# Kernel tuning notes

Hardware: AMD Instinct MI355X
Metric: run time of the kernel (lower is better)

Reference implementation:

```python
import jax, jax.numpy as jnp
import numpy as np

B, S, D, H = 2, 2048, 1024, 16
HD = D // H  # 64
MASK_VAL = -10000.0


def setup_inputs() -> dict:
    key = jax.random.key(0)
    ks = jax.random.split(key, 8)
    sc = 0.02
    q_features = jax.random.normal(ks[0], (B, S, D), jnp.float32)
    kv_features = jax.random.normal(ks[1], (B, S, D), jnp.float32)
    # causal mask, broadcastable (1,1,S,S)
    mask = jnp.tril(jnp.ones((S, S), jnp.bool_))[None, None]
    Wq = jax.random.normal(ks[2], (D, D), jnp.float32) * sc
    bq = jnp.zeros((D,), jnp.float32)
    Wkv = jax.random.normal(ks[3], (D, 2 * D), jnp.float32) * sc
    bkv = jnp.zeros((2 * D,), jnp.float32)
    Wp = jax.random.normal(ks[4], (D, D), jnp.float32) * sc
    bp = jnp.zeros((D,), jnp.float32)
    return {"q_features": q_features, "kv_features": kv_features, "mask": mask,
            "Wq": Wq, "bq": bq, "Wkv": Wkv, "bkv": bkv, "Wp": Wp, "bp": bp}


def _split_heads(t):
    # (B,S,D) -> (B,H,S,HD)
    return t.reshape(B, S, H, HD).transpose(0, 2, 1, 3)


def reference(q_features, kv_features, mask, Wq, bq, Wkv, bkv, Wp, bp):
    query = q_features @ Wq + bq            # (B,S,D)
    kv = kv_features @ Wkv + bkv            # (B,S,2D)
    key, value = jnp.split(kv, 2, axis=-1)
    q = _split_heads(query)                 # (B,H,S,HD)
    k = _split_heads(key)
    v = _split_heads(value)
    scores = jnp.einsum('bhqd,bhkd->bhqk', q, k) / jnp.sqrt(jnp.float32(HD))
    scores = jnp.where(mask, scores, jnp.asarray(MASK_VAL, scores.dtype))
    attn = jax.nn.softmax(scores, axis=-1)  # (B,H,S,S)
    out = jnp.einsum('bhqk,bhkd->bhqd', attn, v)
    out = out.transpose(0, 2, 1, 3).reshape(B, S, D)  # merge heads
    return out @ Wp + bp
```

## Files before the change

kernel.cpp:

```cpp
#include <hip/hip_runtime.h>

typedef unsigned short u16;
typedef unsigned int u32;
typedef __attribute__((ext_vector_type(4))) unsigned short us4;
typedef __attribute__((ext_vector_type(8))) unsigned short us8;
typedef __attribute__((ext_vector_type(4))) short s16x4;
typedef __attribute__((ext_vector_type(8))) __bf16 bf16x8;
typedef __attribute__((ext_vector_type(4))) float floatx4;

#define S_ 2048
#define D_ 1024
#define QSC 0.18033688f

__device__ __forceinline__ float b2f(u16 u) {
  unsigned v = ((unsigned)u) << 16;
  return __builtin_bit_cast(float, v);
}
__device__ __forceinline__ u16 f2bf(float f) {
  unsigned u = __builtin_bit_cast(unsigned, f);
  unsigned r = (u + 0x7fffu + ((u >> 16) & 1u)) >> 16;
  return (u16)r;
}
__device__ __forceinline__ u16 f2bf_rhu(float f) {
  return (u16)((__builtin_bit_cast(unsigned, f) + 0x8000u) >> 16);
}

typedef const __attribute__((address_space(1))) u32* gas_t;
typedef __attribute__((address_space(3))) u32* las_t;
__device__ __forceinline__ void gload16(const u16* g, u16* l) {
  __builtin_amdgcn_global_load_lds((gas_t)g, (las_t)l, 16, 0, 0);
}

#define PBAR()                                   \
  {                                              \
    __builtin_amdgcn_sched_barrier(0);           \
    asm volatile("" ::: "memory");               \
    __builtin_amdgcn_s_barrier();                \
    asm volatile("" ::: "memory");               \
    __builtin_amdgcn_sched_barrier(0);           \
  }
#define WAITVM(N) asm volatile("s_waitcnt vmcnt(" #N ")" ::: "memory")

__global__ __launch_bounds__(256) void prep(
    const float* __restrict__ qf, const float* __restrict__ kvf,
    const float* __restrict__ Wq, const float* __restrict__ Wkv,
    const float* __restrict__ Wp, u16* __restrict__ qa, u16* __restrict__ kva,
    u16* __restrict__ Wqt, u16* __restrict__ Wkvt, u16* __restrict__ Wpt) {
  int bid = blockIdx.x, tid = threadIdx.x;
  if (bid < 4096) {
    const float* src = (bid < 2048) ? qf : kvf;
    u16* dst = (bid < 2048) ? qa : kva;
    size_t i = ((size_t)(bid & 2047) * 256 + tid) * 8;
    floatx4 a = *(const floatx4*)(src + i);
    floatx4 b = *(const floatx4*)(src + i + 4);
    us8 r;
#pragma unroll
    for (int j = 0; j < 4; j++) { r[j] = f2bf(a[j]); r[4 + j] = f2bf(b[j]); }
    *(us8*)(dst + i) = r;
  } else {
    int t = bid - 4096;
    const float* src; u16* dst; int R, C;
    if (t < 1024)      { src = Wq;  dst = Wqt;  R = 1024; C = 1024; }
    else if (t < 3072) { t -= 1024; src = Wkv; dst = Wkvt; R = 1024; C = 2048; }
    else               { t -= 3072; src = Wp;  dst = Wpt;  R = 1024; C = 1024; }
    int bx = t % (C >> 5), by = t / (C >> 5);
    __shared__ u16 tile[32][33];
    int tx = tid & 31, ty = tid >> 5;
    int x = bx * 32 + tx;
    for (int i = ty; i < 32; i += 8)
      tile[i][tx] = f2bf(src[(size_t)(by * 32 + i) * C + x]);
    __syncthreads();
    int ox = by * 32 + tx;
    for (int i = ty; i < 32; i += 8)
      dst[(size_t)(bx * 32 + i) * R + ox] = tile[tx][i];
  }
}

template <int MODE>
__device__ __forceinline__ void gemm256(
    const u16* __restrict__ A, const u16* __restrict__ Bt,
    const float* __restrict__ bias, void* __restrict__ C0,
    u16* __restrict__ C1, int N, int m0, int n0, u16* smem, float cscale) {
  int tid = threadIdx.x;
  int w = tid >> 6, lane = tid & 63;
  int quad = lane >> 4, l16 = lane & 15;
  int wr = w >> 2, wc = w & 3;

  int gch = ((lane & 7) ^ ((lane >> 3) & 7)) << 3;
  const u16* Ag = A + (size_t)(m0 + w * 32 + (lane >> 3)) * 1024 + gch;
  const u16* Bg = Bt + (size_t)(n0 + w * 32 + (lane >> 3)) * 1024 + gch;
  u16* Adst = smem + w * 32 * 64;
  u16* Bdst = smem + 32768 + w * 32 * 64;

  int ab = (wr * 128 + l16) * 64;
  int bb = 32768 + (wc * 64 + l16) * 64;
  int xk0 = (quad ^ (l16 & 7)) << 3;
  int xk1 = ((4 + quad) ^ (l16 & 7)) << 3;

  floatx4 acc[8][4] = {};

#define STAGE3(tn, SD)                                                  \
  {                                                                     \
    _Pragma("unroll") for (int i = 0; i < 4; i++) {                     \
      gload16(Ag + (size_t)(tn) * 64 + (size_t)i * 8192,                \
              Adst + (SD) + i * 512);                                   \
      gload16(Bg + (size_t)(tn) * 64 + (size_t)i * 8192,                \
              Bdst + (SD) + i * 512);                                   \
    }                                                                   \
  }

#define COMPUTE3(SOFF)                                                  \
  {                                                                     \
    _Pragma("unroll") for (int kk = 0; kk < 2; kk++) {                  \
      int xk = kk ? xk1 : xk0;                                          \
      bf16x8 bfr[4];                                                    \
      _Pragma("unroll") for (int nf = 0; nf < 4; nf++)                  \
        bfr[nf] = __builtin_bit_cast(bf16x8,                            \
            *(const us8*)&smem[(SOFF) + bb + nf * 1024 + xk]);          \
      _Pragma("unroll") for (int mf = 0; mf < 8; mf++) {                \
        bf16x8 afr = __builtin_bit_cast(bf16x8,                         \
            *(const us8*)&smem[(SOFF) + ab + mf * 1024 + xk]);          \
        _Pragma("unroll") for (int nf = 0; nf < 4; nf++)                \
          acc[mf][nf] = __builtin_amdgcn_mfma_f32_16x16x32_bf16(        \
              afr, bfr[nf], acc[mf][nf], 0, 0, 0);                      \
      }                                                                 \
    }                                                                   \
  }

  STAGE3(0, 0);
  WAITVM(0);
  PBAR();
#pragma unroll 1
  for (int t = 0; t < 16; t += 2) {
    STAGE3(t + 1, 16384);
    COMPUTE3(0);
    WAITVM(0);
    PBAR();
    if (t + 2 < 16) STAGE3(t + 2, 0);
    COMPUTE3(16384);
    WAITVM(0);
    PBAR();
  }

#undef STAGE3
#undef COMPUTE3

#pragma unroll
  for (int mf = 0; mf < 8; mf++) {
#pragma unroll
    for (int nf = 0; nf < 4; nf++) {
      int col = n0 + wc * 64 + nf * 16 + l16;
      int rowq = m0 + wr * 128 + mf * 16 + quad * 4;
      float bv = bias[col];
      if (MODE == 0) {
        u16* o = (u16*)C0;
#pragma unroll
        for (int r = 0; r < 4; r++)
          o[(size_t)(rowq + r) * N + col] = f2bf((acc[mf][nf][r] + bv) * cscale);
      } else {
        if (col < 1024) {
          u16* o = (u16*)C0;
#pragma unroll
          for (int r = 0; r < 4; r++)
            o[(size_t)(rowq + r) * 1024 + col] = f2bf(acc[mf][nf][r] + bv);
        } else {
          int vcol = col - 1024;
          int b = rowq >> 11, s0 = rowq & 2047;
          us4 pv;
#pragma unroll
          for (int r = 0; r < 4; r++) pv[r] = f2bf(acc[mf][nf][r] + bv);
          *(us4*)&C1[((size_t)(b * 1024 + vcol)) * (size_t)S_ + s0] = pv;
        }
      }
    }
  }
}

__global__ __launch_bounds__(512, 2) void gemm_qkv(
    const u16* __restrict__ qa, const u16* __restrict__ kva,
    const u16* __restrict__ Wqt, const u16* __restrict__ Wkvt,
    const float* __restrict__ bq, const float* __restrict__ bkv,
    u16* __restrict__ Qb, u16* __restrict__ Kb, u16* __restrict__ Vt) {
  __shared__ __align__(16) u16 smem[65536];
  int bid = blockIdx.x;
  int work = (bid & 7) * 24 + (bid >> 3);
  if (work < 64) {
    gemm256<0>(qa, Wqt, bq, Qb, nullptr, 1024,
               (work >> 2) * 256, (work & 3) * 256, smem, QSC);
  } else {
    int lb = work - 64;
    gemm256<2>(kva, Wkvt, bkv, Kb, Vt, 2048,
               (lb >> 3) * 256, (lb & 7) * 256, smem, 1.0f);
  }
}

template <int TM, int TN, int MODE>
__device__ __forceinline__ void gemm_core(
    const u16* __restrict__ A, const u16* __restrict__ Bt,
    const float* __restrict__ bias, void* __restrict__ C0,
    u16* __restrict__ C1, int N, int n0, int m0,
    u16* As, u16* Bs, float cscale) {
  constexpr int MT = TM / 32, NT = TN / 32;
  int tid  = threadIdx.x;
  int wave = tid >> 6, lane = tid & 63;
  int quad = lane >> 4, l16 = lane & 15;
  int wr = wave >> 1, wc = wave & 1;
  const u16* Ag = A  + (size_t)(m0 + wave * 8 + (lane >> 3)) * 1024 + (lane & 7) * 8;
  const u16* Bg = Bt + (size_t)(n0 + wave * 8 + (lane >> 3)) * 1024 + (lane & 7) * 8;
  u16* Aw = As + wave * 8 * 64;
  u16* Bw = Bs + wave * 8 * 64;
  floatx4 acc[MT][NT] = {};
  for (int k0 = 0; k0 < 1024; k0 += 64) {
    if (k0) __syncthreads();
#pragma unroll
    for (int p = 0; p < TM / 32; p++)
      gload16(Ag + (size_t)p * 32 * 1024 + k0, Aw + p * 32 * 64);
#pragma unroll
    for (int p = 0; p < TN / 32; p++)
      gload16(Bg + (size_t)p * 32 * 1024 + k0, Bw + p * 32 * 64);
    __syncthreads();
#pragma unroll
    for (int kk = 0; kk < 2; kk++) {
      bf16x8 af[MT], bf[NT];
#pragma unroll
      for (int mt = 0; mt < MT; mt++)
        af[mt] = __builtin_bit_cast(bf16x8,
            *(const us8*)&As[(wr * (TM / 2) + mt * 16 + l16) * 64 + (kk * 4 + quad) * 8]);
#pragma unroll
      for (int nt = 0; nt < NT; nt++)
        bf[nt] = __builtin_bit_cast(bf16x8,
            *(const us8*)&Bs[(wc * (TN / 2) + nt * 16 + l16) * 64 + (kk * 4 + quad) * 8]);
#pragma unroll
      for (int mt = 0; mt < MT; mt++)
#pragma unroll
        for (int nt = 0; nt < NT; nt++)
          acc[mt][nt] = __builtin_amdgcn_mfma_f32_16x16x32_bf16(
              af[mt], bf[nt], acc[mt][nt], 0, 0, 0);
    }
  }
#pragma unroll
  for (int mt = 0; mt < MT; mt++) {
#pragma unroll
    for (int nt = 0; nt < NT; nt++) {
      int col  = n0 + wc * (TN / 2) + nt * 16 + l16;
      int rowq = m0 + wr * (TM / 2) + mt * 16 + quad * 4;
      float bv = bias[col];
      if (MODE == 0) {
        u16* o = (u16*)C0;
#pragma unroll
        for (int r = 0; r < 4; r++)
          o[(size_t)(rowq + r) * N + col] = f2bf((acc[mt][nt][r] + bv) * cscale);
      } else if (MODE == 1) {
        float* o = (float*)C0;
#pragma unroll
        for (int r = 0; r < 4; r++)
          o[(size_t)(rowq + r) * N + col] = acc[mt][nt][r] + bv;
      } else {
        if (col < 1024) {
          u16* o = (u16*)C0;
#pragma unroll
          for (int r = 0; r < 4; r++)
            o[(size_t)(rowq + r) * 1024 + col] = f2bf(acc[mt][nt][r] + bv);
        } else {
          int vcol = col - 1024;
          int b = rowq >> 11, s0 = rowq & 2047;
          us4 pv;
#pragma unroll
          for (int r = 0; r < 4; r++) pv[r] = f2bf(acc[mt][nt][r] + bv);
          *(us4*)&C1[((size_t)(b * 1024 + vcol)) * (size_t)S_ + s0] = pv;
        }
      }
    }
  }
}

__global__ __launch_bounds__(256) void gemm_out(
    const u16* __restrict__ AO, const u16* __restrict__ Wpt,
    const float* __restrict__ bp, float* __restrict__ out) {
  __shared__ __align__(16) u16 As[64 * 64];
  __shared__ __align__(16) u16 Bs[128 * 64];
  int work = (blockIdx.x & 7) * 64 + (blockIdx.x >> 3);
  gemm_core<64, 128, 1>(AO, Wpt, bp, out, nullptr, 1024,
                        (work & 7) * 128, (work >> 3) * 64, As, Bs, 1.0f);
}

__global__ __launch_bounds__(512) void attn_fwd(
    const u16* __restrict__ Q, const u16* __restrict__ Kb,
    const u16* __restrict__ Vt, u16* __restrict__ O,
    u16* __restrict__ Opart, float* __restrict__ ml) {
  __shared__ __align__(16) u16 sm[16384];
  int tid  = threadIdx.x;
  int w    = tid >> 6, lane = tid & 63;
  int quad = lane >> 4, l16 = lane & 15;
  int bh = blockIdx.x, b = bh >> 4, h = bh & 15;
  int y = blockIdx.y;

  static const signed char yt_[24] = {15,15,7,14,14,13,13,6,12,12,11,11,5,
                                      10,10,9,9,4,8,8,3,2,1,0};
  static const signed char yh_[24] = {0,1,-1,0,1,0,1,-1,0,1,0,1,-1,
                                      0,1,0,1,-1,0,1,-1,-1,-1,-1};
  int t = yt_[y], hh = yh_[y];
  bool split = hh >= 0;
  int kb0, kb1;
  if (split) { kb0 = hh ? (t + 1) : 0; kb1 = hh ? (2 * t + 2) : (t + 1); }
  else       { kb0 = 0; kb1 = 2 * t + 2; }
  int n = kb1 - kb0;

  const size_t row0 = (size_t)b * S_;
  const u16* Kg = Kb + row0 * D_ + h * 64;
  const u16* Vg = Vt + ((size_t)b * 1024 + h * 64) * S_;

  int qlo = t * 128 + w * 16;
  int dkb = qlo >> 6;
  int qg  = (qlo & 63) + l16;

  const u16* qp = Q + (row0 + qlo + l16) * D_ + h * 64 + quad * 8;
  bf16x8 aqv[2];
  aqv[0] = __builtin_bit_cast(bf16x8, *(const us8*)(qp));
  aqv[1] = __builtin_bit_cast(bf16x8, *(const us8*)(qp + 32));

  floatx4 o_[4] = {};
  floatx4 l_acc = {};
  const s16x4 ones4 = {0x3F80, 0x3F80, 0x3F80, 0x3F80};

  int srow = tid >> 3, c8 = tid & 7;
  int woff = srow * 64 + ((c8 ^ (srow & 7)) << 3);
  u16* smK = sm;
  u16* smV = sm + 8192;

  const u16* Kp = Kg + (size_t)(kb0 * 64 + srow) * D_ + c8 * 8;
  const u16* Vp = Vg + (size_t)srow * S_ + kb0 * 64 + c8 * 8;
  us8 pk = *(const us8*)Kp, pv = *(const us8*)Vp;
  *(us8*)&smK[woff] = pk;
  *(us8*)&smV[woff] = pv;
  if (n > 1) {
    Kp += (size_t)64 * D_; Vp += 64;
    pk = *(const us8*)Kp; pv = *(const us8*)Vp;
  }
  __syncthreads();

  for (int i = 0; i < n; i++) {
    int cur = i & 1;
    int kb = kb0 + i;
    if (i + 1 < n) {
      int nxt = (cur ^ 1) * 4096;
      *(us8*)&smK[nxt + woff] = pk;
      *(us8*)&smV[nxt + woff] = pv;
      if (i + 2 < n) {
        Kp += (size_t)64 * D_; Vp += 64;
        pk = *(const us8*)Kp; pv = *(const us8*)Vp;
      }
    }
    if (kb <= dkb) {
      const u16* Ksb = smK + cur * 4096;
      const u16* Vsb = smV + cur * 4096;

      floatx4 s[4] = {};
      __builtin_amdgcn_s_setprio(1);
#pragma unroll
      for (int kk = 0; kk < 2; kk++)
#pragma unroll
        for (int nt = 0; nt < 4; nt++) {
          us8 kf = *(const us8*)&Ksb[(nt * 16 + l16) * 64 +
                                     (((kk * 4 + quad) ^ (l16 & 7)) << 3)];
          s[nt] = __builtin_amdgcn_mfma_f32_16x16x32_bf16(
              __builtin_bit_cast(bf16x8, kf), aqv[kk], s[nt], 0, 0, 0);
        }
      __builtin_amdgcn_s_setprio(0);

      if (kb == dkb) {
#pragma unroll
        for (int nt = 0; nt < 4; nt++)
#pragma unroll
          for (int r = 0; r < 4; r++)
            if (nt * 16 + quad * 4 + r > qg) s[nt][r] = -1e5f;
      }

      s16x4 pb[4];
#pragma unroll
      for (int nt = 0; nt < 4; nt++)
#pragma unroll
        for (int r = 0; r < 4; r++)
          pb[nt][r] = (short)f2bf_rhu(__builtin_amdgcn_exp2f(s[nt][r]));

      __builtin_amdgcn_s_setprio(1);
#pragma unroll
      for (int nt = 0; nt < 4; nt++) {
        l_acc = __builtin_amdgcn_mfma_f32_16x16x16bf16_1k(ones4, pb[nt], l_acc, 0, 0, 0);
#pragma unroll
        for (int mt = 0; mt < 4; mt++) {
          int hd = mt * 16 + l16;
          int chunk = nt * 2 + (quad >> 1);
          us4 vf = *(const us4*)&Vsb[hd * 64 + ((chunk ^ (l16 & 7)) << 3) + (quad & 1) * 4];
          o_[mt] = __builtin_amdgcn_mfma_f32_16x16x16bf16_1k(
              __builtin_bit_cast(s16x4, vf), pb[nt], o_[mt], 0, 0, 0);
        }
      }
      __builtin_amdgcn_s_setprio(0);
    }
    __syncthreads();
  }

  if (!split) {
    float rl = __builtin_amdgcn_rcpf(l_acc[0]);
    size_t orow = (row0 + qlo + l16) * D_ + h * 64;
#pragma unroll
    for (int mt = 0; mt < 4; mt++) {
      us4 ov;
#pragma unroll
      for (int r = 0; r < 4; r++) ov[r] = f2bf(o_[mt][r] * rl);
      *(us4*)&O[orow + mt * 16 + quad * 4] = ov;
    }
  } else {
    int part = (t - 8) * 2 + hh;
    u16* op = Opart + ((size_t)(bh * 16 + part)) * 8192;
    int rloc = w * 16 + l16;
#pragma unroll
    for (int mt = 0; mt < 4; mt++) {
      us4 ov;
#pragma unroll
      for (int r = 0; r < 4; r++) ov[r] = f2bf(o_[mt][r]);
      *(us4*)&op[rloc * 64 + mt * 16 + quad * 4] = ov;
    }
    if (quad == 0)
      ml[(size_t)(bh * 16 + part) * 128 + rloc] = l_acc[0];
  }
}

__global__ __launch_bounds__(256) void combine(
    const u16* __restrict__ Opart, const float* __restrict__ ml,
    u16* __restrict__ O) {
  int bh = blockIdx.x, b = bh >> 4, h = bh & 15;
  int t = 8 + blockIdx.y;
  int p0 = bh * 16 + (t - 8) * 2;
  const u16* o1 = Opart + (size_t)p0 * 8192;
  const u16* o2 = o1 + 8192;
  int row = threadIdx.x >> 1, ch = (threadIdx.x & 1) * 32;
  float l1 = ml[(size_t)p0 * 128 + row];
  float l2 = ml[(size_t)(p0 + 1) * 128 + row];
  float inv = __builtin_amdgcn_rcpf(l1 + l2);
  size_t orow = ((size_t)b * S_ + t * 128 + row) * D_ + h * 64 + ch;
#pragma unroll
  for (int v = 0; v < 4; v++) {
    us8 x1 = *(const us8*)&o1[row * 64 + ch + v * 8];
    us8 x2 = *(const us8*)&o2[row * 64 + ch + v * 8];
    us8 out;
#pragma unroll
    for (int j = 0; j < 8; j++)
      out[j] = f2bf((b2f(x1[j]) + b2f(x2[j])) * inv);
    *(us8*)&O[orow + v * 8] = out;
  }
}

extern "C" void kernel_launch(void* const* d_in, const int* in_sizes, int n_in,
                              void* d_out, int out_size, void* d_ws, size_t ws_size,
                              hipStream_t stream) {
  const float* qf  = (const float*)d_in[0];
  const float* kvf = (const float*)d_in[1];
  const float* Wq  = (const float*)d_in[3];
  const float* bq  = (const float*)d_in[4];
  const float* Wkv = (const float*)d_in[5];
  const float* bkv = (const float*)d_in[6];
  const float* Wp  = (const float*)d_in[7];
  const float* bp  = (const float*)d_in[8];

  char* ws = (char*)d_ws;
  const size_t MB = 1048576;
  u16*   kva  = (u16*)(ws);
  u16*   AO   = (u16*)(ws);
  u16*   Kbp  = (u16*)(ws + 8 * MB);
  u16*   Vtp  = (u16*)(ws + 16 * MB);
  u16*   Wqt  = (u16*)(ws + 24 * MB);
  float* mlp  = (float*)(ws + 24 * MB);
  u16*   Wkvt = (u16*)(ws + 26 * MB);
  u16*   Wpt  = (u16*)(ws + 30 * MB);
  u16*   qa    = (u16*)d_out;
  u16*   Opart = (u16*)d_out;
  u16*   Qb    = (u16*)d_out + (size_t)4 * 1048576;

  prep<<<8192, 256, 0, stream>>>(qf, kvf, Wq, Wkv, Wp, qa, kva, Wqt, Wkvt, Wpt);
  gemm_qkv<<<192, 512, 0, stream>>>(qa, kva, Wqt, Wkvt, bq, bkv, Qb, Kbp, Vtp);
  attn_fwd<<<dim3(32, 24), 512, 0, stream>>>(Qb, Kbp, Vtp, AO, Opart, mlp);
  combine<<<dim3(32, 8), 256, 0, stream>>>(Opart, mlp, AO);
  gemm_out<<<512, 256, 0, stream>>>(AO, Wpt, bp, (float*)d_out);
}
```

Measured before the change: 211.0 us.

## Use 4-wave double-buffered swizzled GEMM with smaller tiles for QKV and output

Replaces the 256x256 8-wave QKV GEMM with a templated 4-wave 128x128 double-buffered swizzled kernel, which gives 768 blocks instead of 192 so more CUs are busy. The output projection moves from the simple single-buffered gemm_core to the same pipelined kernel with 128x64 tiles. The weight transpose in prep now writes 4-element vector stores. Smaller tiles reduce data reuse per block and raise global traffic, in exchange for better occupancy and load balance.

```diff
diff --git a/kernel.cpp b/kernel.cpp
--- a/kernel.cpp
+++ b/kernel.cpp
@@ -70,93 +70,103 @@
     for (int i = ty; i < 32; i += 8)
       tile[i][tx] = f2bf(src[(size_t)(by * 32 + i) * C + x]);
     __syncthreads();
-    int ox = by * 32 + tx;
-    for (int i = ty; i < 32; i += 8)
-      dst[(size_t)(bx * 32 + i) * R + ox] = tile[tx][i];
-  }
-}
-
-template <int MODE>
-__device__ __forceinline__ void gemm256(
+    int r = tid >> 3, c4 = tid & 7;
+    us4 v;
+#pragma unroll
+    for (int j = 0; j < 4; j++) v[j] = tile[c4 * 4 + j][r];
+    *(us4*)&dst[(size_t)(bx * 32 + r) * R + by * 32 + c4 * 4] = v;
+  }
+}
+
+template <int TM, int TN, int MODE>
+__device__ __forceinline__ void gemm4w(
     const u16* __restrict__ A, const u16* __restrict__ Bt,
     const float* __restrict__ bias, void* __restrict__ C0,
     u16* __restrict__ C1, int N, int m0, int n0, u16* smem, float cscale) {
+  constexpr int MF = TM / 32, NF = TN / 32;
+  constexpr int ASZ = TM * 64;
+  constexpr int SLOT = (TM + TN) * 64;
   int tid = threadIdx.x;
   int w = tid >> 6, lane = tid & 63;
   int quad = lane >> 4, l16 = lane & 15;
-  int wr = w >> 2, wc = w & 3;
+  int wr = w >> 1, wc = w & 1;
 
   int gch = ((lane & 7) ^ ((lane >> 3) & 7)) << 3;
-  const u16* Ag = A + (size_t)(m0 + w * 32 + (lane >> 3)) * 1024 + gch;
-  const u16* Bg = Bt + (size_t)(n0 + w * 32 + (lane >> 3)) * 1024 + gch;
-  u16* Adst = smem + w * 32 * 64;
-  u16* Bdst = smem + 32768 + w * 32 * 64;
-
-  int ab = (wr * 128 + l16) * 64;
-  int bb = 32768 + (wc * 64 + l16) * 64;
+  const u16* Ag = A + (size_t)(m0 + w * (TM / 4) + (lane >> 3)) * 1024 + gch;
+  const u16* Bg = Bt + (size_t)(n0 + w * (TN / 4) + (lane >> 3)) * 1024 + gch;
+  u16* Adst = smem + w * (TM / 4) * 64;
+  u16* Bdst = smem + ASZ + w * (TN / 4) * 64;
+
+  int ab = (wr * (TM / 2) + l16) * 64;
+  int bb = ASZ + (wc * (TN / 2) + l16) * 64;
   int xk0 = (quad ^ (l16 & 7)) << 3;
   int xk1 = ((4 + quad) ^ (l16 & 7)) << 3;
 
-  floatx4 acc[8][4] = {};
-
-#define STAGE3(tn, SD)                                                  \
+  floatx4 acc[MF][NF] = {};
+
+#define STAGE4(tn, s_)                                                  \
   {                                                                     \
-    _Pragma("unroll") for (int i = 0; i < 4; i++) {                     \
+    _Pragma("unroll") for (int i = 0; i < MF; i++)                      \
       gload16(Ag + (size_t)(tn) * 64 + (size_t)i * 8192,                \
-              Adst + (SD) + i * 512);                                   \
+              Adst + (s_) * SLOT + i * 512);                            \
+    _Pragma("unroll") for (int i = 0; i < NF; i++)                      \
       gload16(Bg + (size_t)(tn) * 64 + (size_t)i * 8192,                \
-              Bdst + (SD) + i * 512);                                   \
-    }                                                                   \
-  }
-
-#define COMPUTE3(SOFF)                                                  \
+              Bdst + (s_) * SLOT + i * 512);                            \
+  }
+
+#define COMPUTE4(SOFF)                                                  \
   {                                                                     \
     _Pragma("unroll") for (int kk = 0; kk < 2; kk++) {                  \
       int xk = kk ? xk1 : xk0;                                          \
-      bf16x8 bfr[4];                                                    \
-      _Pragma("unroll") for (int nf = 0; nf < 4; nf++)                  \
+      bf16x8 bfr[NF];                                                   \
+      _Pragma("unroll") for (int nf = 0; nf < NF; nf++)                 \
         bfr[nf] = __builtin_bit_cast(bf16x8,                            \
             *(const us8*)&smem[(SOFF) + bb + nf * 1024 + xk]);          \
-      _Pragma("unroll") for (int mf = 0; mf < 8; mf++) {                \
+      _Pragma("unroll") for (int mf = 0; mf < MF; mf++) {               \
         bf16x8 afr = __builtin_bit_cast(bf16x8,                         \
             *(const us8*)&smem[(SOFF) + ab + mf * 1024 + xk]);          \
-        _Pragma("unroll") for (int nf = 0; nf < 4; nf++)                \
+        _Pragma("unroll") for (int nf = 0; nf < NF; nf++)               \
           acc[mf][nf] = __builtin_amdgcn_mfma_f32_16x16x32_bf16(        \
               afr, bfr[nf], acc[mf][nf], 0, 0, 0);                      \
       }                                                                 \
     }                                                                   \
   }
 
-  STAGE3(0, 0);
+  STAGE4(0, 0);
   WAITVM(0);
   PBAR();
 #pragma unroll 1
   for (int t = 0; t < 16; t += 2) {
-    STAGE3(t + 1, 16384);
-    COMPUTE3(0);
+    STAGE4(t + 1, 1);
+    COMPUTE4(0);
     WAITVM(0);
     PBAR();
-    if (t + 2 < 16) STAGE3(t + 2, 0);
-    COMPUTE3(16384);
+    if (t + 2 < 16) STAGE4(t + 2, 0);
+    COMPUTE4(SLOT);
     WAITVM(0);
     PBAR();
   }
 
-#undef STAGE3
-#undef COMPUTE3
-
-#pragma unroll
-  for (int mf = 0; mf < 8; mf++) {
-#pragma unroll
-    for (int nf = 0; nf < 4; nf++) {
-      int col = n0 + wc * 64 + nf * 16 + l16;
-      int rowq = m0 + wr * 128 + mf * 16 + quad * 4;
+#undef STAGE4
+#undef COMPUTE4
+
+#pragma unroll
+  for (int mf = 0; mf < MF; mf++) {
+#pragma unroll
+    for (int nf = 0; nf < NF; nf++) {
+      int col = n0 + wc * (TN / 2) + nf * 16 + l16;
+      int rowq = m0 + wr * (TM / 2) + mf * 16 + quad * 4;
       float bv = bias[col];
       if (MODE == 0) {
         u16* o = (u16*)C0;
 #pragma unroll
         for (int r = 0; r < 4; r++)
           o[(size_t)(rowq + r) * N + col] = f2bf((acc[mf][nf][r] + bv) * cscale);
+      } else if (MODE == 1) {
+        float* o = (float*)C0;
+#pragma unroll
+        for (int r = 0; r < 4; r++)
+          o[(size_t)(rowq + r) * N + col] = acc[mf][nf][r] + bv;
       } else {
         if (col < 1024) {
           u16* o = (u16*)C0;
@@ -176,112 +186,31 @@
   }
 }
 
-__global__ __launch_bounds__(512, 2) void gemm_qkv(
+__global__ __launch_bounds__(256, 2) void gemm_qkv(
     const u16* __restrict__ qa, const u16* __restrict__ kva,
     const u16* __restrict__ Wqt, const u16* __restrict__ Wkvt,
     const float* __restrict__ bq, const float* __restrict__ bkv,
     u16* __restrict__ Qb, u16* __restrict__ Kb, u16* __restrict__ Vt) {
-  __shared__ __align__(16) u16 smem[65536];
+  __shared__ __align__(16) u16 smem[32768];
   int bid = blockIdx.x;
-  int work = (bid & 7) * 24 + (bid >> 3);
-  if (work < 64) {
-    gemm256<0>(qa, Wqt, bq, Qb, nullptr, 1024,
-               (work >> 2) * 256, (work & 3) * 256, smem, QSC);
+  int work = (bid & 7) * 96 + (bid >> 3);
+  if (work < 256) {
+    gemm4w<128, 128, 0>(qa, Wqt, bq, Qb, nullptr, 1024,
+                        (work >> 3) * 128, (work & 7) * 128, smem, QSC);
   } else {
-    int lb = work - 64;
-    gemm256<2>(kva, Wkvt, bkv, Kb, Vt, 2048,
-               (lb >> 3) * 256, (lb & 7) * 256, smem, 1.0f);
-  }
-}
-
-template <int TM, int TN, int MODE>
-__device__ __forceinline__ void gemm_core(
-    const u16* __restrict__ A, const u16* __restrict__ Bt,
-    const float* __restrict__ bias, void* __restrict__ C0,
-    u16* __restrict__ C1, int N, int n0, int m0,
-    u16* As, u16* Bs, float cscale) {
-  constexpr int MT = TM / 32, NT = TN / 32;
-  int tid  = threadIdx.x;
-  int wave = tid >> 6, lane = tid & 63;
-  int quad = lane >> 4, l16 = lane & 15;
-  int wr = wave >> 1, wc = wave & 1;
-  const u16* Ag = A  + (size_t)(m0 + wave * 8 + (lane >> 3)) * 1024 + (lane & 7) * 8;
-  const u16* Bg = Bt + (size_t)(n0 + wave * 8 + (lane >> 3)) * 1024 + (lane & 7) * 8;
-  u16* Aw = As + wave * 8 * 64;
-  u16* Bw = Bs + wave * 8 * 64;
-  floatx4 acc[MT][NT] = {};
-  for (int k0 = 0; k0 < 1024; k0 += 64) {
-    if (k0) __syncthreads();
-#pragma unroll
-    for (int p = 0; p < TM / 32; p++)
-      gload16(Ag + (size_t)p * 32 * 1024 + k0, Aw + p * 32 * 64);
-#pragma unroll
-    for (int p = 0; p < TN / 32; p++)
-      gload16(Bg + (size_t)p * 32 * 1024 + k0, Bw + p * 32 * 64);
-    __syncthreads();
-#pragma unroll
-    for (int kk = 0; kk < 2; kk++) {
-      bf16x8 af[MT], bf[NT];
-#pragma unroll
-      for (int mt = 0; mt < MT; mt++)
-        af[mt] = __builtin_bit_cast(bf16x8,
-            *(const us8*)&As[(wr * (TM / 2) + mt * 16 + l16) * 64 + (kk * 4 + quad) * 8]);
-#pragma unroll
-      for (int nt = 0; nt < NT; nt++)
-        bf[nt] = __builtin_bit_cast(bf16x8,
-            *(const us8*)&Bs[(wc * (TN / 2) + nt * 16 + l16) * 64 + (kk * 4 + quad) * 8]);
-#pragma unroll
-      for (int mt = 0; mt < MT; mt++)
-#pragma unroll
-        for (int nt = 0; nt < NT; nt++)
-          acc[mt][nt] = __builtin_amdgcn_mfma_f32_16x16x32_bf16(
-              af[mt], bf[nt], acc[mt][nt], 0, 0, 0);
-    }
-  }
-#pragma unroll
-  for (int mt = 0; mt < MT; mt++) {
-#pragma unroll
-    for (int nt = 0; nt < NT; nt++) {
-      int col  = n0 + wc * (TN / 2) + nt * 16 + l16;
-      int rowq = m0 + wr * (TM / 2) + mt * 16 + quad * 4;
-      float bv = bias[col];
-      if (MODE == 0) {
-        u16* o = (u16*)C0;
-#pragma unroll
-        for (int r = 0; r < 4; r++)
-          o[(size_t)(rowq + r) * N + col] = f2bf((acc[mt][nt][r] + bv) * cscale);
-      } else if (MODE == 1) {
-        float* o = (float*)C0;
-#pragma unroll
-        for (int r = 0; r < 4; r++)
-          o[(size_t)(rowq + r) * N + col] = acc[mt][nt][r] + bv;
-      } else {
-        if (col < 1024) {
-          u16* o = (u16*)C0;
-#pragma unroll
-          for (int r = 0; r < 4; r++)
-            o[(size_t)(rowq + r) * 1024 + col] = f2bf(acc[mt][nt][r] + bv);
-        } else {
-          int vcol = col - 1024;
-          int b = rowq >> 11, s0 = rowq & 2047;
-          us4 pv;
-#pragma unroll
-          for (int r = 0; r < 4; r++) pv[r] = f2bf(acc[mt][nt][r] + bv);
-          *(us4*)&C1[((size_t)(b * 1024 + vcol)) * (size_t)S_ + s0] = pv;
-        }
-      }
-    }
-  }
-}
-
-__global__ __launch_bounds__(256) void gemm_out(
+    int lb = work - 256;
+    gemm4w<128, 128, 2>(kva, Wkvt, bkv, Kb, Vt, 2048,
+                        (lb >> 4) * 128, (lb & 15) * 128, smem, 1.0f);
+  }
+}
+
+__global__ __launch_bounds__(256, 3) void gemm_out(
     const u16* __restrict__ AO, const u16* __restrict__ Wpt,
     const float* __restrict__ bp, float* __restrict__ out) {
-  __shared__ __align__(16) u16 As[64 * 64];
-  __shared__ __align__(16) u16 Bs[128 * 64];
+  __shared__ __align__(16) u16 smem[24576];
   int work = (blockIdx.x & 7) * 64 + (blockIdx.x >> 3);
-  gemm_core<64, 128, 1>(AO, Wpt, bp, out, nullptr, 1024,
-                        (work & 7) * 128, (work >> 3) * 64, As, Bs, 1.0f);
+  gemm4w<128, 64, 1>(AO, Wpt, bp, out, nullptr, 1024,
+                     (work >> 4) * 128, (work & 15) * 64, smem, 1.0f);
 }
 
 __global__ __launch_bounds__(512) void attn_fwd(
@@ -479,7 +408,7 @@
   u16*   Qb    = (u16*)d_out + (size_t)4 * 1048576;
 
   prep<<<8192, 256, 0, stream>>>(qf, kvf, Wq, Wkv, Wp, qa, kva, Wqt, Wkvt, Wpt);
-  gemm_qkv<<<192, 512, 0, stream>>>(qa, kva, Wqt, Wkvt, bq, bkv, Qb, Kbp, Vtp);
+  gemm_qkv<<<768, 256, 0, stream>>>(qa, kva, Wqt, Wkvt, bq, bkv, Qb, Kbp, Vtp);
   attn_fwd<<<dim3(32, 24), 512, 0, stream>>>(Qb, Kbp, Vtp, AO, Opart, mlp);
   combine<<<dim3(32, 8), 256, 0, stream>>>(Opart, mlp, AO);
   gemm_out<<<512, 256, 0, stream>>>(AO, Wpt, bp, (float*)d_out);
```

After: 204.2 us. -3.2%, faster.
